# Kernel tuning notes

Hardware: AMD Instinct MI355X
Metric: run time of the kernel (lower is better)

## Reference

```python
import jax, jax.numpy as jnp
import numpy as np

B, H, W, C = 8, 256, 256, 128  # batch, grid-H, grid-W, channel width
MODES = 16
SCALE = 1.0 / (C * C)  # 1/(in_width*out_width)


def _corner_mask(h, w, f):
    # mask truncates the FIRST two axes of w_ft (as in the original code),
    # keeping the full rfft axis.
    m = np.zeros((h, w, f), dtype=np.float32)
    m[:MODES, :MODES, :] = 1.0
    m[-MODES:, :MODES, :] = 1.0
    m[:MODES, -MODES:, :] = 1.0
    m[-MODES:, -MODES:, :] = 1.0
    return jnp.asarray(m)


def setup_inputs() -> dict:
    key = jax.random.key(0)
    k1, k2 = jax.random.split(key)
    x = jax.random.normal(k1, (B, H, W, C), dtype=jnp.float32)
    w = SCALE * jax.random.uniform(k2, (H, W, C), dtype=jnp.float32)
    b = jnp.zeros((H, W, C), dtype=jnp.float32)
    return {"x": x, "w": w, "b": b}


def reference(x, w, b):
    # rfft2d over the innermost two dims (W, C), matching tf.signal.rfft2d
    x_ft = jnp.fft.rfft2(x, axes=(-2, -1))   # [B, H, W, C//2+1] complex
    w_ft = jnp.fft.rfft2(w, axes=(-2, -1))   # [H, W, C//2+1]
    b_ft = jnp.fft.rfft2(b, axes=(-2, -1))
    xw_ft = x_ft * w_ft + b_ft               # broadcast over batch
    mask = _corner_mask(*w_ft.shape)         # corners along axes (0,1)
    xw_ft = xw_ft * mask
    # irfft2d with default sizes recovers last dim = 2*(C//2+1-1) = C
    return jnp.fft.irfft2(xw_ft, axes=(-2, -1))
```

## Files before the change

### kernel.cpp

```cpp
#include <hip/hip_runtime.h>

#define TPK 512
#define TPA 1024
#define NF0 256
#define NF2 1536

typedef float f4v __attribute__((ext_vector_type(4)));

__device__ __forceinline__ int br7(int k) {
  return (int)(__brev((unsigned int)k) >> 25);
}

template <int NT>
__device__ __forceinline__ void zero_fill_slab(float* __restrict__ out,
                                               int zi, int tid) {
  const int zb = zi / 224;
  const int zh = 16 + (zi - zb * 224);
  f4v* o4 = (f4v*)(out + ((size_t)(zb * 256 + zh)) * 32768);
  const f4v z = {0.f, 0.f, 0.f, 0.f};
  #pragma unroll
  for (int i = 0; i < 8192 / NT; ++i)
    __builtin_nontemporal_store(z, &o4[tid + i * NT]);
}

__device__ __forceinline__ void fft16_pos(float* ar, float* ai) {
  constexpr float TC[4][8] = {
    {1.f, 0.f, 0.f, 0.f, 0.f, 0.f, 0.f, 0.f},
    {1.f, 0.f, 0.f, 0.f, 0.f, 0.f, 0.f, 0.f},
    {1.f, 0.70710678f, 0.f, -0.70710678f, 0.f, 0.f, 0.f, 0.f},
    {1.f, 0.92387953f, 0.70710678f, 0.38268343f, 0.f, -0.38268343f, -0.70710678f, -0.92387953f}
  };
  constexpr float TS[4][8] = {
    {0.f, 0.f, 0.f, 0.f, 0.f, 0.f, 0.f, 0.f},
    {0.f, 1.f, 0.f, 0.f, 0.f, 0.f, 0.f, 0.f},
    {0.f, 0.70710678f, 1.f, 0.70710678f, 0.f, 0.f, 0.f, 0.f},
    {0.f, 0.38268343f, 0.70710678f, 0.92387953f, 1.f, 0.92387953f, 0.70710678f, 0.38268343f}
  };
  #pragma unroll
  for (int s = 0; s < 4; ++s) {
    const int L = 1 << s;
    #pragma unroll
    for (int jj = 0; jj < 8; ++jj) {
      if (jj < L) {
        const float tc = TC[s][jj], ts = TS[s][jj];
        #pragma unroll
        for (int i0 = jj; i0 < 16; i0 += 2 * L) {
          const float xr = ar[i0 + L], xi = ai[i0 + L];
          const float pr = xr * tc - xi * ts;
          const float pi = xr * ts + xi * tc;
          const float qr = ar[i0], qi = ai[i0];
          ar[i0 + L] = qr - pr; ai[i0 + L] = qi - pi;
          ar[i0]     = qr + pr; ai[i0]     = qi + pi;
        }
      }
    }
  }
}

template <int TPBv>
__device__ void phaseA_reduce(const float* __restrict__ src,
                              float (*XR)[128], float (*XI)[128],
                              float (*SR)[128], float (*SI)[128],
                              const float* Rc, const float* Rs, int tid) {
  constexpr int NQ = TPBv / 128;
  constexpr int JN = 16 / NQ;
  const int c = tid & 127;
  const int q = tid >> 7;

  constexpr float C16[16] = {1.f, 0.92387953f, 0.70710678f, 0.38268343f, 0.f,
                             -0.38268343f, -0.70710678f, -0.92387953f, -1.f,
                             -0.92387953f, -0.70710678f, -0.38268343f, 0.f,
                             0.38268343f, 0.70710678f, 0.92387953f};
  constexpr float S16[16] = {0.f, 0.38268343f, 0.70710678f, 0.92387953f, 1.f,
                             0.92387953f, 0.70710678f, 0.38268343f, 0.f,
                             -0.38268343f, -0.70710678f, -0.92387953f, -1.f,
                             -0.92387953f, -0.70710678f, -0.38268343f};

  float accR[17], accI[17];
  #pragma unroll
  for (int f = 0; f < 17; ++f) { accR[f] = 0.f; accI[f] = 0.f; }

  #pragma unroll
  for (int j = 0; j < JN; ++j) {
    const int w0 = q * JN + j;
    float xv[16];
    #pragma unroll
    for (int w1 = 0; w1 < 16; ++w1)
      xv[w1] = src[(w1 * 16 + w0) * 128 + c];
    float SRe[9], SIm[9];
    #pragma unroll
    for (int g = 0; g < 9; ++g) {
      float sr = 0.f, si = 0.f;
      #pragma unroll
      for (int w1 = 0; w1 < 16; ++w1) {
        const int m = (g * w1) & 15;
        sr = fmaf(xv[w1], C16[m], sr);
        si = fmaf(xv[w1], -S16[m], si);
      }
      SRe[g] = sr; SIm[g] = si;
    }
    #pragma unroll
    for (int f = 0; f < 17; ++f) {
      const int g = f & 15;
      const float sr = (g <= 8) ? SRe[g] : SRe[16 - g];
      const float si = (g <= 8) ? SIm[g] : -SIm[16 - g];
      const int idx = (f * w0) & 255;
      const float tc = Rc[idx], ts = -Rs[idx];
      accR[f] = fmaf(sr, tc, fmaf(-si, ts, accR[f]));
      accI[f] = fmaf(sr, ts, fmaf(si, tc, accI[f]));
    }
  }
  #pragma unroll
  for (int r = 0; r < NQ / 2; ++r) {
    if (q == 2 * r) {
      if (r == 0) {
        #pragma unroll
        for (int f = 0; f < 17; ++f) { XR[f][c] = accR[f]; XI[f][c] = accI[f]; }
      } else {
        #pragma unroll
        for (int f = 0; f < 17; ++f) { XR[f][c] += accR[f]; XI[f][c] += accI[f]; }
      }
    } else if (q == 2 * r + 1) {
      if (r == 0) {
        #pragma unroll
        for (int f = 0; f < 17; ++f) { SR[f][c] = accR[f]; SI[f][c] = accI[f]; }
      } else {
        #pragma unroll
        for (int f = 0; f < 17; ++f) { SR[f][c] += accR[f]; SI[f][c] += accI[f]; }
      }
    }
    __syncthreads();
  }
  for (int u = tid; u < 17 * 128; u += TPBv) {
    const int row = u >> 7, cc = u & 127;
    XR[row][cc] += SR[row][cc];
    XI[row][cc] += SI[row][cc];
  }
  __syncthreads();
}

template <int TPBv>
__device__ void fftc17_lds(float (*XR)[128], float (*XI)[128],
                           const float* Rc, const float* Rs, int tid) {
  for (int s = 6; s >= 0; --s) {
    const int L = 1 << s;
    for (int u = tid; u < 17 * 64; u += TPBv) {
      const int row = u >> 6, qq = u & 63;
      const int jj = qq & (L - 1);
      const int pos = ((qq >> s) << (s + 1)) | jj;
      const int ti = jj << (7 - s);
      const float tc = Rc[ti], ts = Rs[ti];
      const float a0r = XR[row][pos],     a0i = XI[row][pos];
      const float b0r = XR[row][pos + L], b0i = XI[row][pos + L];
      XR[row][pos] = a0r + b0r; XI[row][pos] = a0i + b0i;
      const float dr = a0r - b0r, di = a0i - b0i;
      XR[row][pos + L] = fmaf(dr, tc, di * ts);
      XI[row][pos + L] = fmaf(di, tc, -dr * ts);
    }
    __syncthreads();
  }
}

__global__ __launch_bounds__(TPK) void k0_wft_and_fill(
    const float* __restrict__ wp, const float* __restrict__ bp,
    float2* __restrict__ wsW, float2* __restrict__ wsB,
    float* __restrict__ out) {
  const int bid = blockIdx.x;
  const int tid = threadIdx.x;
  if (bid >= 64) {
    zero_fill_slab<TPK>(out, bid - 64, tid);
    return;
  }
  __shared__ float XR[17][128], XI[17][128];
  __shared__ float SR[17][128], SI[17][128];
  __shared__ float Rc[256], Rs[256];
  for (int i = tid; i < 256; i += TPK) {
    float sv, cv; sincosf(6.283185307179586f * (float)i / 256.0f, &sv, &cv);
    Rc[i] = cv; Rs[i] = sv;
  }
  __syncthreads();
  const int which = bid >> 5;
  const int ha = bid & 31;
  const int h = (ha < 16) ? ha : (224 + ha);
  const float* src = (which ? bp : wp) + (size_t)h * 32768;
  phaseA_reduce<TPK>(src, XR, XI, SR, SI, Rc, Rs, tid);
  fftc17_lds<TPK>(XR, XI, Rc, Rs, tid);
  float2* dst = which ? wsB : wsW;
  for (int u = tid; u < 32 * 65; u += TPK) {
    const int fi = u / 65, k = u - fi * 65;
    const int f = fi - 16;
    float xr, xi;
    if (f >= 0) { const int p = br7(k); xr = XR[f][p]; xi = XI[f][p]; }
    else { const int kk = (128 - k) & 127; const int p = br7(kk);
           xr = XR[-f][p]; xi = -XI[-f][p]; }
    dst[(ha * 32 + fi) * 65 + k] = make_float2(xr, xi);
  }
}

__global__ __launch_bounds__(TPA) void fourier_active(
    const float* __restrict__ x, const float2* __restrict__ wsW,
    const float2* __restrict__ wsB, float* __restrict__ out) {
  const int bid = blockIdx.x;
  const int tid = threadIdx.x;
  if (bid >= 256) {
    zero_fill_slab<TPA>(out, NF0 + (bid - 256), tid);
    return;
  }
  __shared__ float XR[17][128], XI[17][128];
  __shared__ float TR[32][128], TI[32][128];
  __shared__ float Rc[256], Rs[256];
  for (int i = tid; i < 256; i += TPA) {
    float sv, cv; sincosf(6.283185307179586f * (float)i / 256.0f, &sv, &cv);
    Rc[i] = cv; Rs[i] = sv;
  }
  __syncthreads();

  const int b = bid >> 5;
  const int ha = bid & 31;
  const int h = (ha < 16) ? ha : (224 + ha);
  const float* src = x + ((size_t)(b * 256 + h)) * 32768;
  phaseA_reduce<TPA>(src, XR, XI, (float(*)[128])TR, (float(*)[128])TI,
                     Rc, Rs, tid);

  const int wid = tid >> 6, lane = tid & 63;
  const int i0 = lane, i1 = lane + 64;

  for (int row = wid; row < 17; row += 16) {
    float ar0 = XR[row][i0], ai0 = XI[row][i0];
    float ar1 = XR[row][i1], ai1 = XI[row][i1];
    {
      const float tc = Rc[2 * lane], ts = Rs[2 * lane];
      const float sr = ar0 - ar1, si = ai0 - ai1;
      ar0 += ar1; ai0 += ai1;
      ar1 = fmaf(sr, tc,  si * ts);
      ai1 = fmaf(si, tc, -sr * ts);
    }
    #pragma unroll
    for (int s = 5; s >= 0; --s) {
      const int L = 1 << s;
      const int m2 = (lane & (L - 1)) << (7 - s);
      const float wc = Rc[m2], wsn = Rs[m2];
      const bool hi = (lane & L) != 0;
      const float br0 = __shfl_xor(ar0, L), bi0 = __shfl_xor(ai0, L);
      const float br1 = __shfl_xor(ar1, L), bi1 = __shfl_xor(ai1, L);
      float dr0 = hi ? (br0 - ar0) : (ar0 + br0);
      float di0 = hi ? (bi0 - ai0) : (ai0 + bi0);
      float dr1 = hi ? (br1 - ar1) : (ar1 + br1);
      float di1 = hi ? (bi1 - ai1) : (ai1 + bi1);
      if (hi) {
        const float t0 = fmaf(dr0, wc,  di0 * wsn);
        di0 = fmaf(di0, wc, -dr0 * wsn); dr0 = t0;
        const float t1 = fmaf(dr1, wc,  di1 * wsn);
        di1 = fmaf(di1, wc, -dr1 * wsn); dr1 = t1;
      }
      ar0 = dr0; ai0 = di0; ar1 = dr1; ai1 = di1;
    }
    XR[row][i0] = ar0; XI[row][i0] = ai0;
    XR[row][i1] = ar1; XI[row][i1] = ai1;
  }
  __syncthreads();

  const int k0 = br7(i0);
  const int k1 = k0 + 1;
  #pragma unroll
  for (int rr = 0; rr < 2; ++rr) {
    int fi; float xr0, xi0, xr1, xi1;
    if (rr == 0) {
      fi = wid + 16;
      xr0 = XR[wid][i0]; xi0 = XI[wid][i0];
      xr1 = XR[wid][i1]; xi1 = XI[wid][i1];
    } else {
      fi = wid;
      const int mrow = 16 - wid;
      const int pm0 = br7((128 - k0) & 127);
      const int pm1 = br7((128 - k1) & 127);
      xr0 = XR[mrow][pm0]; xi0 = -XI[mrow][pm0];
      xr1 = XR[mrow][pm1]; xi1 = -XI[mrow][pm1];
    }
    float gr0 = 0.f, gi0 = 0.f, gr1 = 0.f, gi1 = 0.f;
    const float2* wrow = &wsW[(ha * 32 + fi) * 65];
    const float2* brow = &wsB[(ha * 32 + fi) * 65];
    if (k0 <= 64) {
      const float2 wf = wrow[k0], bf = brow[k0];
      const float al = (k0 == 0 || k0 == 64) ? 1.f : 2.f;
      gr0 = al * (xr0 * wf.x - xi0 * wf.y + bf.x);
      gi0 = al * (xr0 * wf.y + xi0 * wf.x + bf.y);
    }
    if (k1 <= 64) {
      const float2 wf = wrow[k1], bf = brow[k1];
      gr1 = 2.f * (xr1 * wf.x - xi1 * wf.y + bf.x);
      gi1 = 2.f * (xr1 * wf.y + xi1 * wf.x + bf.y);
    }
    #pragma unroll
    for (int s = 0; s <= 5; ++s) {
      const int L = 1 << s;
      const int m2 = (lane & (L - 1)) << (7 - s);
      const float wc = Rc[m2], wsn = Rs[m2];
      const bool hi = (lane & L) != 0;
      const float br0 = __shfl_xor(gr0, L), bi0 = __shfl_xor(gi0, L);
      const float br1 = __shfl_xor(gr1, L), bi1 = __shfl_xor(gi1, L);
      const float q0ri = hi ? gr0 : br0, q0ii = hi ? gi0 : bi0;
      const float q1ri = hi ? gr1 : br1, q1ii = hi ? gi1 : bi1;
      const float q0r = fmaf(q0ri, wc, -q0ii * wsn);
      const float q0i = fmaf(q0ii, wc,  q0ri * wsn);
      const float q1r = fmaf(q1ri, wc, -q1ii * wsn);
      const float q1i = fmaf(q1ii, wc,  q1ri * wsn);
      const float p0r = hi ? br0 : gr0, p0i = hi ? bi0 : gi0;
      const float p1r = hi ? br1 : gr1, p1i = hi ? bi1 : gi1;
      gr0 = hi ? (p0r - q0r) : (p0r + q0r);
      gi0 = hi ? (p0i - q0i) : (p0i + q0i);
      gr1 = hi ? (p1r - q1r) : (p1r + q1r);
      gi1 = hi ? (p1i - q1i) : (p1i + q1i);
    }
    {
      const float wc = Rc[2 * lane], wsn = Rs[2 * lane];
      const float qr = fmaf(gr1, wc, -gi1 * wsn);
      const float qi = fmaf(gi1, wc,  gr1 * wsn);
      gr1 = gr0 - qr; gi1 = gi0 - qi;
      gr0 = gr0 + qr; gi0 = gi0 + qi;
    }
    TR[fi][i0] = gr0; TI[fi][i0] = gi0;
    TR[fi][i1] = gr1; TI[fi][i1] = gi1;
  }
  __syncthreads();

  const int c = tid & 127;
  const int q = tid >> 7;
  constexpr int BR4[16] = {0, 8, 4, 12, 2, 10, 6, 14, 1, 9, 5, 13, 3, 11, 7, 15};
  const float inv = 1.0f / 32768.0f;
  float* og = out + ((size_t)(b * 256 + h)) * 32768;

  #pragma unroll 1
  for (int it = 0; it < 2; ++it) {
    const int w0 = q + it * 8;
    float Ur[16], Ui[16];
    #pragma unroll
    for (int g = 0; g < 16; ++g) {
      const int gb = BR4[g];
      const float t1r = TR[gb + 16][c], t1i = TI[gb + 16][c];
      const float t0r = TR[gb][c],      t0i = TI[gb][c];
      const int iw1 = (gb * w0) & 255;
      const int iw2 = ((gb - 16) * w0) & 255;
      const float c1 = Rc[iw1], s1 = Rs[iw1];
      const float c2 = Rc[iw2], s2 = Rs[iw2];
      Ur[g] = t1r * c1 - t1i * s1 + t0r * c2 - t0i * s2;
      Ui[g] = t1r * s1 + t1i * c1 + t0r * s2 + t0i * c2;
    }
    fft16_pos(Ur, Ui);
    #pragma unroll
    for (int w1 = 0; w1 < 16; ++w1)
      og[(w1 * 16 + w0) * 128 + c] = Ur[w1] * inv;
  }
}

extern "C" void kernel_launch(void* const* d_in, const int* in_sizes, int n_in,
                              void* d_out, int out_size, void* d_ws, size_t ws_size,
                              hipStream_t stream) {
  const float* x = (const float*)d_in[0];
  const float* w = (const float*)d_in[1];
  const float* b = (const float*)d_in[2];
  float* out = (float*)d_out;
  float2* wsW = (float2*)d_ws;
  float2* wsB = wsW + 32 * 32 * 65;

  hipLaunchKernelGGL(k0_wft_and_fill, dim3(64 + NF0), dim3(TPK), 0, stream,
                     w, b, wsW, wsB, out);
  hipLaunchKernelGGL(fourier_active, dim3(256 + NF2), dim3(TPA), 0, stream,
                     x, wsW, wsB, out);
}
```

Measured before the change: 78.45 us.

## Move all zero-fill into fourier kernel and gate fill blocks on x-read counter

All zero-filling of the inactive output rows moves out of the weight-FFT kernel, which shrinks to its 64 compute blocks. The zero-fill is handled by 256 extra blocks in the main kernel, each writing seven slabs. Those fill blocks spin on a global atomic counter, with a bounded number of sleeps, until the active blocks have finished reading their x rows. This aims to keep the fill writes from competing for bandwidth with the x reads. It adds atomic traffic and a bounded busy-wait, and with only 40 iterations the ordering is a heuristic rather than a guarantee.

```diff
diff --git a/kernel.cpp b/kernel.cpp
--- a/kernel.cpp
+++ b/kernel.cpp
@@ -2,25 +2,11 @@
 
 #define TPK 512
 #define TPA 1024
-#define NF0 256
-#define NF2 1536
 
 typedef float f4v __attribute__((ext_vector_type(4)));
 
 __device__ __forceinline__ int br7(int k) {
   return (int)(__brev((unsigned int)k) >> 25);
-}
-
-template <int NT>
-__device__ __forceinline__ void zero_fill_slab(float* __restrict__ out,
-                                               int zi, int tid) {
-  const int zb = zi / 224;
-  const int zh = 16 + (zi - zb * 224);
-  f4v* o4 = (f4v*)(out + ((size_t)(zb * 256 + zh)) * 32768);
-  const f4v z = {0.f, 0.f, 0.f, 0.f};
-  #pragma unroll
-  for (int i = 0; i < 8192 / NT; ++i)
-    __builtin_nontemporal_store(z, &o4[tid + i * NT]);
 }
 
 __device__ __forceinline__ void fft16_pos(float* ar, float* ai) {
@@ -161,16 +147,14 @@
   }
 }
 
-__global__ __launch_bounds__(TPK) void k0_wft_and_fill(
+__global__ __launch_bounds__(TPK) void k0_wft(
     const float* __restrict__ wp, const float* __restrict__ bp,
     float2* __restrict__ wsW, float2* __restrict__ wsB,
-    float* __restrict__ out) {
+    unsigned int* __restrict__ ctr) {
   const int bid = blockIdx.x;
   const int tid = threadIdx.x;
-  if (bid >= 64) {
-    zero_fill_slab<TPK>(out, bid - 64, tid);
-    return;
-  }
+  if (bid == 0 && tid == 0)
+    __hip_atomic_store(ctr, 0u, __ATOMIC_RELAXED, __HIP_MEMORY_SCOPE_AGENT);
   __shared__ float XR[17][128], XI[17][128];
   __shared__ float SR[17][128], SI[17][128];
   __shared__ float Rc[256], Rs[256];
@@ -199,13 +183,36 @@
 
 __global__ __launch_bounds__(TPA) void fourier_active(
     const float* __restrict__ x, const float2* __restrict__ wsW,
-    const float2* __restrict__ wsB, float* __restrict__ out) {
+    const float2* __restrict__ wsB, float* __restrict__ out,
+    unsigned int* __restrict__ ctr) {
   const int bid = blockIdx.x;
   const int tid = threadIdx.x;
+
   if (bid >= 256) {
-    zero_fill_slab<TPA>(out, NF0 + (bid - 256), tid);
+    if (tid == 0) {
+      for (int it = 0; it < 40; ++it) {
+        const unsigned int v =
+            __hip_atomic_load(ctr, __ATOMIC_RELAXED, __HIP_MEMORY_SCOPE_AGENT);
+        if (v >= 256u) break;
+        __builtin_amdgcn_s_sleep(16);
+      }
+    }
+    __syncthreads();
+    const int pid = bid - 256;
+    const f4v z = {0.f, 0.f, 0.f, 0.f};
+    #pragma unroll 1
+    for (int s = 0; s < 7; ++s) {
+      const int zi = pid * 7 + s;
+      const int zb = zi / 224;
+      const int zh = 16 + (zi - zb * 224);
+      f4v* o4 = (f4v*)(out + ((size_t)(zb * 256 + zh)) * 32768);
+      #pragma unroll
+      for (int i = 0; i < 8; ++i)
+        __builtin_nontemporal_store(z, &o4[tid + i * 1024]);
+    }
     return;
   }
+
   __shared__ float XR[17][128], XI[17][128];
   __shared__ float TR[32][128], TI[32][128];
   __shared__ float Rc[256], Rs[256];
@@ -221,6 +228,8 @@
   const float* src = x + ((size_t)(b * 256 + h)) * 32768;
   phaseA_reduce<TPA>(src, XR, XI, (float(*)[128])TR, (float(*)[128])TI,
                      Rc, Rs, tid);
+  if (tid == 0)
+    __hip_atomic_fetch_add(ctr, 1u, __ATOMIC_RELAXED, __HIP_MEMORY_SCOPE_AGENT);
 
   const int wid = tid >> 6, lane = tid & 63;
   const int i0 = lane, i1 = lane + 64;
@@ -362,9 +371,10 @@
   float* out = (float*)d_out;
   float2* wsW = (float2*)d_ws;
   float2* wsB = wsW + 32 * 32 * 65;
-
-  hipLaunchKernelGGL(k0_wft_and_fill, dim3(64 + NF0), dim3(TPK), 0, stream,
-                     w, b, wsW, wsB, out);
-  hipLaunchKernelGGL(fourier_active, dim3(256 + NF2), dim3(TPA), 0, stream,
-                     x, wsW, wsB, out);
-}
+  unsigned int* ctr = (unsigned int*)(wsB + 32 * 32 * 65);
+
+  hipLaunchKernelGGL(k0_wft, dim3(64), dim3(TPK), 0, stream,
+                     w, b, wsW, wsB, ctr);
+  hipLaunchKernelGGL(fourier_active, dim3(512), dim3(TPA), 0, stream,
+                     x, wsW, wsB, out, ctr);
+}
```

Result: slower. 81.01 us (+3.3%).
